# Kernel optimization log

Hardware: AMD Instinct MI355X
Metric: run time of the kernel (lower is better)

## Reference

```python
import jax, jax.numpy as jnp
import numpy as np

EPS = 1e-6

def _feature_map(x):
    # elu(x) + 1 == where(x > 0, x + 1, exp(x))
    return jnp.where(x > 0, x + 1.0, jnp.exp(x))

def setup_inputs() -> dict:
    key = jax.random.key(0)
    kq, kk, kv = jax.random.split(key, 3)
    B, H, L, D = 4, 16, 8192, 64
    q = jax.random.normal(kq, (B, H, L, D), dtype=jnp.float32)
    k = jax.random.normal(kk, (B, H, L, D), dtype=jnp.float32)
    v = jax.random.normal(kv, (B, H, L, D), dtype=jnp.float32)
    attention_mask = jnp.ones((B, L), dtype=jnp.float32)
    return {"q": q, "k": k, "v": v, "attention_mask": attention_mask}

def reference(q, k, v, attention_mask):
    # feature-mapped queries/keys (compute_scores)
    q = _feature_map(q)
    k = _feature_map(k)
    # mask keys/values: mask shape [B,L] -> [B,1,L,1]
    mask = attention_mask[:, None, :, None]
    k = k * mask
    v = v * mask
    # causal branch: cumulative sums along sequence dim
    k_cumsum = jnp.cumsum(k, axis=2)            # [B,H,L,D]
    kv_cumsum = jnp.cumsum(k * v, axis=2)       # [B,H,L,D]
    z = jnp.einsum('bhld,bhld->bhl', q, k_cumsum) + EPS
    z = z * attention_mask[:, None, :]
    output = q * kv_cumsum                       # einsum 'bhld,bhld->bhld' is elementwise
    output = output / z[..., None]
    return output
```

## Files before the change

### kernel.cpp

```cpp
#include <hip/hip_runtime.h>
#include <cstdint>

#define EPS 1e-6f

constexpr int Bsz = 4, Hn = 16, Lseq = 8192, Dd = 64;
constexpr int BH = Bsz * Hn;
constexpr int CHUNK = 128;
constexpr int CPB = Lseq / CHUNK;
constexpr int NCHUNKS = BH * CPB;
constexpr int WPB = 4;

__device__ __forceinline__ float phi(float x) {
    return x > 0.0f ? x + 1.0f : __expf(x);
}

__global__ __launch_bounds__(256) void partials_kernel(
    const float* __restrict__ k, const float* __restrict__ v,
    const float* __restrict__ mask,
    float* __restrict__ pk, float* __restrict__ pkv)
{
    const int wave = blockIdx.x * WPB + (threadIdx.x >> 6);
    const int lane = threadIdx.x & 63;
    const int rg = lane >> 4;
    const int dg = lane & 15;
    const int bh = wave / CPB;
    const int c  = wave % CPB;
    const int b  = bh / Hn;
    const int l0 = c * CHUNK;

    float4 ak  = make_float4(0.f, 0.f, 0.f, 0.f);
    float4 akv = make_float4(0.f, 0.f, 0.f, 0.f);

    for (int i = 0; i < CHUNK; i += 4) {
        const int l = l0 + i + rg;
        const size_t off = ((size_t)bh * Lseq + l) * Dd + dg * 4;
        const float4 k4 = *(const float4*)(k + off);
        const float4 v4 = *(const float4*)(v + off);
        const float m = mask[(size_t)b * Lseq + l];
        float t;
        t = phi(k4.x) * m; ak.x += t; akv.x += t * (v4.x * m);
        t = phi(k4.y) * m; ak.y += t; akv.y += t * (v4.y * m);
        t = phi(k4.z) * m; ak.z += t; akv.z += t * (v4.z * m);
        t = phi(k4.w) * m; ak.w += t; akv.w += t * (v4.w * m);
    }

    #pragma unroll
    for (int off = 16; off <= 32; off <<= 1) {
        ak.x  += __shfl_xor(ak.x,  off, 64);
        ak.y  += __shfl_xor(ak.y,  off, 64);
        ak.z  += __shfl_xor(ak.z,  off, 64);
        ak.w  += __shfl_xor(ak.w,  off, 64);
        akv.x += __shfl_xor(akv.x, off, 64);
        akv.y += __shfl_xor(akv.y, off, 64);
        akv.z += __shfl_xor(akv.z, off, 64);
        akv.w += __shfl_xor(akv.w, off, 64);
    }

    if (rg == 0) {
        const size_t o = (size_t)wave * Dd + dg * 4;
        *(float4*)(pk  + o) = ak;
        *(float4*)(pkv + o) = akv;
    }
}

__global__ __launch_bounds__(64) void scan_kernel(
    float* __restrict__ pk, float* __restrict__ pkv)
{
    const int bh = blockIdx.x;
    const int d  = threadIdx.x;
    float rk = 0.f, rkv = 0.f;
    for (int c = 0; c < CPB; ++c) {
        const size_t o = ((size_t)(bh * CPB + c)) * Dd + d;
        const float tk = pk[o], tkv = pkv[o];
        pk[o]  = rk;  rk  += tk;
        pkv[o] = rkv; rkv += tkv;
    }
}

__global__ __launch_bounds__(256) void final_kernel(
    const float* __restrict__ q, const float* __restrict__ k,
    const float* __restrict__ v, const float* __restrict__ mask,
    const float* __restrict__ pk, const float* __restrict__ pkv,
    float* __restrict__ out)
{
    const int wave = blockIdx.x * WPB + (threadIdx.x >> 6);
    const int lane = threadIdx.x & 63;
    const int rg = lane >> 4;
    const int dg = lane & 15;
    const int bh = wave / CPB;
    const int c  = wave % CPB;
    const int b  = bh / Hn;
    const int l0 = c * CHUNK;

    const size_t po = (size_t)wave * Dd + dg * 4;
    float4 Sk  = *(const float4*)(pk  + po);
    float4 Skv = *(const float4*)(pkv + po);

    for (int i = 0; i < CHUNK; i += 4) {
        const int l = l0 + i + rg;
        const size_t off = ((size_t)bh * Lseq + l) * Dd + dg * 4;
        const float4 q4 = *(const float4*)(q + off);
        const float4 k4 = *(const float4*)(k + off);
        const float4 v4 = *(const float4*)(v + off);
        const float m = mask[(size_t)b * Lseq + l];

        float4 fq, a, akv;
        fq.x = phi(q4.x); fq.y = phi(q4.y); fq.z = phi(q4.z); fq.w = phi(q4.w);
        a.x = phi(k4.x) * m; akv.x = a.x * (v4.x * m);
        a.y = phi(k4.y) * m; akv.y = a.y * (v4.y * m);
        a.z = phi(k4.z) * m; akv.z = a.z * (v4.z * m);
        a.w = phi(k4.w) * m; akv.w = a.w * (v4.w * m);

        float t;
        t = __shfl_up(a.x,  16, 64); if (rg >= 1) a.x  += t;
        t = __shfl_up(a.y,  16, 64); if (rg >= 1) a.y  += t;
        t = __shfl_up(a.z,  16, 64); if (rg >= 1) a.z  += t;
        t = __shfl_up(a.w,  16, 64); if (rg >= 1) a.w  += t;
        t = __shfl_up(akv.x,16, 64); if (rg >= 1) akv.x += t;
        t = __shfl_up(akv.y,16, 64); if (rg >= 1) akv.y += t;
        t = __shfl_up(akv.z,16, 64); if (rg >= 1) akv.z += t;
        t = __shfl_up(akv.w,16, 64); if (rg >= 1) akv.w += t;
        t = __shfl_up(a.x,  32, 64); if (rg >= 2) a.x  += t;
        t = __shfl_up(a.y,  32, 64); if (rg >= 2) a.y  += t;
        t = __shfl_up(a.z,  32, 64); if (rg >= 2) a.z  += t;
        t = __shfl_up(a.w,  32, 64); if (rg >= 2) a.w  += t;
        t = __shfl_up(akv.x,32, 64); if (rg >= 2) akv.x += t;
        t = __shfl_up(akv.y,32, 64); if (rg >= 2) akv.y += t;
        t = __shfl_up(akv.z,32, 64); if (rg >= 2) akv.z += t;
        t = __shfl_up(akv.w,32, 64); if (rg >= 2) akv.w += t;

        const float4 ik  = make_float4(Sk.x + a.x,  Sk.y + a.y,  Sk.z + a.z,  Sk.w + a.w);
        const float4 ikv = make_float4(Skv.x + akv.x, Skv.y + akv.y, Skv.z + akv.z, Skv.w + akv.w);

        float p = fq.x * ik.x + fq.y * ik.y + fq.z * ik.z + fq.w * ik.w;
        p += __shfl_xor(p, 1, 64);
        p += __shfl_xor(p, 2, 64);
        p += __shfl_xor(p, 4, 64);
        p += __shfl_xor(p, 8, 64);
        const float z = (p + EPS) * m;
        const float inv = 1.0f / z;

        float4 o4;
        o4.x = fq.x * ikv.x * inv;
        o4.y = fq.y * ikv.y * inv;
        o4.z = fq.z * ikv.z * inv;
        o4.w = fq.w * ikv.w * inv;
        *(float4*)(out + off) = o4;

        Sk.x  += __shfl(a.x,  48 + dg, 64);
        Sk.y  += __shfl(a.y,  48 + dg, 64);
        Sk.z  += __shfl(a.z,  48 + dg, 64);
        Sk.w  += __shfl(a.w,  48 + dg, 64);
        Skv.x += __shfl(akv.x, 48 + dg, 64);
        Skv.y += __shfl(akv.y, 48 + dg, 64);
        Skv.z += __shfl(akv.z, 48 + dg, 64);
        Skv.w += __shfl(akv.w, 48 + dg, 64);
    }
}

extern "C" void kernel_launch(void* const* d_in, const int* in_sizes, int n_in,
                              void* d_out, int out_size, void* d_ws, size_t ws_size,
                              hipStream_t stream) {
    const float* q    = (const float*)d_in[0];
    const float* k    = (const float*)d_in[1];
    const float* v    = (const float*)d_in[2];
    const float* mask = (const float*)d_in[3];
    float* out = (float*)d_out;

    float* pk  = (float*)d_ws;
    float* pkv = pk + (size_t)NCHUNKS * Dd;

    partials_kernel<<<NCHUNKS / WPB, 256, 0, stream>>>(k, v, mask, pk, pkv);
    scan_kernel<<<BH, 64, 0, stream>>>(pk, pkv);
    final_kernel<<<NCHUNKS / WPB, 256, 0, stream>>>(q, k, v, mask, pk, pkv, out);
}
```

Baseline: 449.7 us.

## Halve chunk size and parallelize scan across four wave segments

Chunk size drops from 128 to 64 rows, doubling the number of waves in the partial and final kernels so each wave's serial loop is shorter and more work is in flight. The scan kernel now uses 256 threads per head, with each of four waves scanning a quarter of the chunks in registers and combining offsets through shared memory, instead of one 64-thread serial loop over all chunks. The partial loop also gets an unroll pragma. The cost is twice as much workspace traffic for the partial sums and a scan that still processes twice as many chunks.

```diff
diff --git a/kernel.cpp b/kernel.cpp
--- a/kernel.cpp
+++ b/kernel.cpp
@@ -5,10 +5,12 @@
 
 constexpr int Bsz = 4, Hn = 16, Lseq = 8192, Dd = 64;
 constexpr int BH = Bsz * Hn;
-constexpr int CHUNK = 128;
+constexpr int CHUNK = 64;
 constexpr int CPB = Lseq / CHUNK;
 constexpr int NCHUNKS = BH * CPB;
 constexpr int WPB = 4;
+constexpr int NBLK = NCHUNKS / WPB;
+constexpr int QCH = CPB / 4;
 
 __device__ __forceinline__ float phi(float x) {
     return x > 0.0f ? x + 1.0f : __expf(x);
@@ -31,6 +33,7 @@
     float4 ak  = make_float4(0.f, 0.f, 0.f, 0.f);
     float4 akv = make_float4(0.f, 0.f, 0.f, 0.f);
 
+    #pragma unroll 4
     for (int i = 0; i < CHUNK; i += 4) {
         const int l = l0 + i + rg;
         const size_t off = ((size_t)bh * Lseq + l) * Dd + dg * 4;
@@ -45,15 +48,15 @@
     }
 
     #pragma unroll
-    for (int off = 16; off <= 32; off <<= 1) {
-        ak.x  += __shfl_xor(ak.x,  off, 64);
-        ak.y  += __shfl_xor(ak.y,  off, 64);
-        ak.z  += __shfl_xor(ak.z,  off, 64);
-        ak.w  += __shfl_xor(ak.w,  off, 64);
-        akv.x += __shfl_xor(akv.x, off, 64);
-        akv.y += __shfl_xor(akv.y, off, 64);
-        akv.z += __shfl_xor(akv.z, off, 64);
-        akv.w += __shfl_xor(akv.w, off, 64);
+    for (int o = 16; o <= 32; o <<= 1) {
+        ak.x  += __shfl_xor(ak.x,  o, 64);
+        ak.y  += __shfl_xor(ak.y,  o, 64);
+        ak.z  += __shfl_xor(ak.z,  o, 64);
+        ak.w  += __shfl_xor(ak.w,  o, 64);
+        akv.x += __shfl_xor(akv.x, o, 64);
+        akv.y += __shfl_xor(akv.y, o, 64);
+        akv.z += __shfl_xor(akv.z, o, 64);
+        akv.w += __shfl_xor(akv.w, o, 64);
     }
 
     if (rg == 0) {
@@ -63,17 +66,42 @@
     }
 }
 
-__global__ __launch_bounds__(64) void scan_kernel(
+__global__ __launch_bounds__(256) void scan_kernel(
     float* __restrict__ pk, float* __restrict__ pkv)
 {
     const int bh = blockIdx.x;
-    const int d  = threadIdx.x;
-    float rk = 0.f, rkv = 0.f;
-    for (int c = 0; c < CPB; ++c) {
-        const size_t o = ((size_t)(bh * CPB + c)) * Dd + d;
-        const float tk = pk[o], tkv = pkv[o];
-        pk[o]  = rk;  rk  += tk;
-        pkv[o] = rkv; rkv += tkv;
+    const int d  = threadIdx.x & 63;
+    const int qc = threadIdx.x >> 6;
+    const size_t base = ((size_t)bh * CPB + qc * QCH) * Dd + d;
+
+    float vk[QCH], vkv[QCH];
+    #pragma unroll
+    for (int j = 0; j < QCH; ++j) {
+        vk[j]  = pk [base + (size_t)j * Dd];
+        vkv[j] = pkv[base + (size_t)j * Dd];
+    }
+
+    float sk = 0.f, skv = 0.f;
+    #pragma unroll
+    for (int j = 0; j < QCH; ++j) {
+        const float tk = vk[j], tkv = vkv[j];
+        vk[j] = sk;   sk  += tk;
+        vkv[j] = skv; skv += tkv;
+    }
+
+    __shared__ float tK[4][64], tKV[4][64];
+    tK[qc][d] = sk; tKV[qc][d] = skv;
+    __syncthreads();
+    float offk = 0.f, offkv = 0.f;
+    #pragma unroll
+    for (int t = 0; t < 3; ++t) {
+        if (t < qc) { offk += tK[t][d]; offkv += tKV[t][d]; }
+    }
+
+    #pragma unroll
+    for (int j = 0; j < QCH; ++j) {
+        pk [base + (size_t)j * Dd] = vk[j]  + offk;
+        pkv[base + (size_t)j * Dd] = vkv[j] + offkv;
     }
 }
 
@@ -104,33 +132,33 @@
         const float4 v4 = *(const float4*)(v + off);
         const float m = mask[(size_t)b * Lseq + l];
 
-        float4 fq, a, akv;
+        float4 fq, a, av;
         fq.x = phi(q4.x); fq.y = phi(q4.y); fq.z = phi(q4.z); fq.w = phi(q4.w);
-        a.x = phi(k4.x) * m; akv.x = a.x * (v4.x * m);
-        a.y = phi(k4.y) * m; akv.y = a.y * (v4.y * m);
-        a.z = phi(k4.z) * m; akv.z = a.z * (v4.z * m);
-        a.w = phi(k4.w) * m; akv.w = a.w * (v4.w * m);
+        a.x = phi(k4.x) * m; av.x = a.x * (v4.x * m);
+        a.y = phi(k4.y) * m; av.y = a.y * (v4.y * m);
+        a.z = phi(k4.z) * m; av.z = a.z * (v4.z * m);
+        a.w = phi(k4.w) * m; av.w = a.w * (v4.w * m);
 
         float t;
         t = __shfl_up(a.x,  16, 64); if (rg >= 1) a.x  += t;
         t = __shfl_up(a.y,  16, 64); if (rg >= 1) a.y  += t;
         t = __shfl_up(a.z,  16, 64); if (rg >= 1) a.z  += t;
         t = __shfl_up(a.w,  16, 64); if (rg >= 1) a.w  += t;
-        t = __shfl_up(akv.x,16, 64); if (rg >= 1) akv.x += t;
-        t = __shfl_up(akv.y,16, 64); if (rg >= 1) akv.y += t;
-        t = __shfl_up(akv.z,16, 64); if (rg >= 1) akv.z += t;
-        t = __shfl_up(akv.w,16, 64); if (rg >= 1) akv.w += t;
+        t = __shfl_up(av.x, 16, 64); if (rg >= 1) av.x += t;
+        t = __shfl_up(av.y, 16, 64); if (rg >= 1) av.y += t;
+        t = __shfl_up(av.z, 16, 64); if (rg >= 1) av.z += t;
+        t = __shfl_up(av.w, 16, 64); if (rg >= 1) av.w += t;
         t = __shfl_up(a.x,  32, 64); if (rg >= 2) a.x  += t;
         t = __shfl_up(a.y,  32, 64); if (rg >= 2) a.y  += t;
         t = __shfl_up(a.z,  32, 64); if (rg >= 2) a.z  += t;
         t = __shfl_up(a.w,  32, 64); if (rg >= 2) a.w  += t;
-        t = __shfl_up(akv.x,32, 64); if (rg >= 2) akv.x += t;
-        t = __shfl_up(akv.y,32, 64); if (rg >= 2) akv.y += t;
-        t = __shfl_up(akv.z,32, 64); if (rg >= 2) akv.z += t;
-        t = __shfl_up(akv.w,32, 64); if (rg >= 2) akv.w += t;
-
-        const float4 ik  = make_float4(Sk.x + a.x,  Sk.y + a.y,  Sk.z + a.z,  Sk.w + a.w);
-        const float4 ikv = make_float4(Skv.x + akv.x, Skv.y + akv.y, Skv.z + akv.z, Skv.w + akv.w);
+        t = __shfl_up(av.x, 32, 64); if (rg >= 2) av.x += t;
+        t = __shfl_up(av.y, 32, 64); if (rg >= 2) av.y += t;
+        t = __shfl_up(av.z, 32, 64); if (rg >= 2) av.z += t;
+        t = __shfl_up(av.w, 32, 64); if (rg >= 2) av.w += t;
+
+        const float4 ik  = make_float4(Sk.x + a.x,   Sk.y + a.y,   Sk.z + a.z,   Sk.w + a.w);
+        const float4 ikv = make_float4(Skv.x + av.x, Skv.y + av.y, Skv.z + av.z, Skv.w + av.w);
 
         float p = fq.x * ik.x + fq.y * ik.y + fq.z * ik.z + fq.w * ik.w;
         p += __shfl_xor(p, 1, 64);
@@ -151,10 +179,10 @@
         Sk.y  += __shfl(a.y,  48 + dg, 64);
         Sk.z  += __shfl(a.z,  48 + dg, 64);
         Sk.w  += __shfl(a.w,  48 + dg, 64);
-        Skv.x += __shfl(akv.x, 48 + dg, 64);
-        Skv.y += __shfl(akv.y, 48 + dg, 64);
-        Skv.z += __shfl(akv.z, 48 + dg, 64);
-        Skv.w += __shfl(akv.w, 48 + dg, 64);
+        Skv.x += __shfl(av.x, 48 + dg, 64);
+        Skv.y += __shfl(av.y, 48 + dg, 64);
+        Skv.z += __shfl(av.z, 48 + dg, 64);
+        Skv.w += __shfl(av.w, 48 + dg, 64);
     }
 }
 
@@ -170,7 +198,7 @@
     float* pk  = (float*)d_ws;
     float* pkv = pk + (size_t)NCHUNKS * Dd;
 
-    partials_kernel<<<NCHUNKS / WPB, 256, 0, stream>>>(k, v, mask, pk, pkv);
-    scan_kernel<<<BH, 64, 0, stream>>>(pk, pkv);
-    final_kernel<<<NCHUNKS / WPB, 256, 0, stream>>>(q, k, v, mask, pk, pkv, out);
-}
+    partials_kernel<<<NBLK, 256, 0, stream>>>(k, v, mask, pk, pkv);
+    scan_kernel<<<BH, 256, 0, stream>>>(pk, pkv);
+    final_kernel<<<NBLK, 256, 0, stream>>>(q, k, v, mask, pk, pkv, out);
+}
```

Result: no change. 451.2 us (+0.3%).
